# Optimization experiments

Hardware: AMD Instinct MI355X
Metric: run time of the kernel (lower is better)

Reference implementation:

```python
import jax, jax.numpy as jnp
import numpy as np
import math

PHI = (1 + math.sqrt(5)) / 2
ALPHA = 1 / PHI          # residual scale
BETA = 1 / PHI ** 2      # sparse-matmul scale
DIM = 1910
NZ = int(DIM * DIM / PHI)


def setup_inputs() -> dict:
    key = jax.random.key(0)
    kx, ki, kv = jax.random.split(key, 3)
    x = jax.random.normal(kx, (8, 4096, DIM), dtype=jnp.float32)
    W_indices = jax.random.randint(ki, (2, NZ), 0, DIM, dtype=jnp.int32)
    W_values = jax.random.normal(kv, (NZ,), dtype=jnp.float32) / math.sqrt(DIM)
    return {"x": x, "W_indices": W_indices, "W_values": W_values}


def reference(x, W_indices, W_values):
    dim = x.shape[-1]
    # COO -> dense: duplicate (row,col) entries sum, matching torch.sparse semantics.
    W = jnp.zeros((dim, dim), dtype=x.dtype).at[W_indices[0], W_indices[1]].add(W_values)
    orig_shape = x.shape
    xf = x.reshape(-1, dim)          # [tokens, dim]
    Wx = xf @ W.T                    # (W @ x.T).T == x @ W.T
    out = ALPHA * xf + BETA * Wx
    return out.reshape(orig_shape)
```

## Files before the change

### kernel.cpp

```cpp
#include <hip/hip_runtime.h>
#include <hip/hip_bf16.h>
#include <stdint.h>

#define DIMV 1910
#define KP   1920
#define NT   30
#define PHI_F  1.6180339887498949f
#define BETA_F 0.3819660112501051f

typedef __attribute__((ext_vector_type(4))) float f32x4;
typedef __attribute__((ext_vector_type(8))) short bf16x8;
typedef __attribute__((ext_vector_type(8))) unsigned short u16x8;

__device__ __forceinline__ void gl16(const void* g, void* l) {
    __builtin_amdgcn_global_load_lds(
        (const __attribute__((address_space(1))) void*)(uintptr_t)g,
        (__attribute__((address_space(3))) void*)(uint32_t)(uintptr_t)l,
        16, 0, 0);
}

__global__ void k_scatter(const int* __restrict__ ridx, const int* __restrict__ cidx,
                          const float* __restrict__ vals, float* __restrict__ Wd, int nz) {
    int i = blockIdx.x * 256 + threadIdx.x;
    if (i < nz) atomicAdd(Wd + (long)ridx[i] * DIMV + cidx[i], vals[i]);
}

__global__ void k_build_w(const float* __restrict__ Wd, unsigned short* __restrict__ Wb, int total8) {
    int stride = gridDim.x * blockDim.x;
    for (int i = blockIdx.x * blockDim.x + threadIdx.x; i < total8; i += stride) {
        int v = i * 8;
        int n = v / KP;
        int k = v - n * KP;
        u16x8 o;
#pragma unroll
        for (int j = 0; j < 8; ++j) {
            int kk = k + j;
            float fv = (n < DIMV && kk < DIMV) ? Wd[(size_t)n * DIMV + kk] : 0.f;
            if (kk == n && n < DIMV) fv += PHI_F;
            __hip_bfloat16 b = __float2bfloat16(fv);
            o[j] = *reinterpret_cast<unsigned short*>(&b);
        }
        *(u16x8*)(Wb + (size_t)v) = o;
    }
}

__global__ void k_conv_x(const float* __restrict__ x, unsigned short* __restrict__ xb, int total8) {
    int stride = gridDim.x * blockDim.x;
    for (int i = blockIdx.x * blockDim.x + threadIdx.x; i < total8; i += stride) {
        int v = i * 8;
        int row = v / KP;
        int col = v - row * KP;
        u16x8 o;
        if (col + 8 <= DIMV) {
            const float2* s = (const float2*)(x + (size_t)row * DIMV + col);
            float2 f0 = s[0], f1 = s[1], f2 = s[2], f3 = s[3];
            float f[8] = {f0.x, f0.y, f1.x, f1.y, f2.x, f2.y, f3.x, f3.y};
#pragma unroll
            for (int j = 0; j < 8; ++j) {
                __hip_bfloat16 b = __float2bfloat16(f[j]);
                o[j] = *reinterpret_cast<unsigned short*>(&b);
            }
        } else {
#pragma unroll
            for (int j = 0; j < 8; ++j) {
                int c = col + j;
                float fv = (c < DIMV) ? x[(size_t)row * DIMV + c] : 0.f;
                __hip_bfloat16 b = __float2bfloat16(fv);
                o[j] = *reinterpret_cast<unsigned short*>(&b);
            }
        }
        *(u16x8*)(xb + (size_t)v) = o;
    }
}

__global__ __launch_bounds__(512, 2) void k_gemm(const short* __restrict__ A,
                                                 const short* __restrict__ B,
                                                 float* __restrict__ C) {
    __shared__ char lds[131072];

    const int bid = blockIdx.x;
    const int bn  = bid & 7;
    const int bm  = bid >> 3;

    const int tid = threadIdx.x;
    const int w   = tid >> 6;
    const int l   = tid & 63;
    const int wm  = w >> 2;
    const int wn  = w & 3;
    const int fr  = l & 15;
    const int q   = l >> 4;

    const int    rs   = tid >> 3;
    const size_t KPB  = (size_t)KP * 2;
    const char*  aSrc = (const char*)A + (size_t)(bm * 256 + rs) * KPB + (((tid & 7) ^ (rs & 7)) * 16);
    const char*  bSrc = (const char*)B + (size_t)(bn * 256 + rs) * KPB + (((tid & 7) ^ (rs & 7)) * 16);
    char* stDst = lds + tid * 16;

    const int co0  = ((q    ) ^ (fr & 7)) * 16;
    const int co1  = ((4 + q) ^ (fr & 7)) * 16;
    const int aOff = (wm * 128 + fr) * 128;
    const int bOff = 32768 + (wn * 64 + fr) * 128;

    f32x4 acc[8][4] = {};

#define STAGE_A(tt, bo, s) gl16(aSrc + (size_t)(s) * 64 * KPB + (size_t)(tt) * 128, stDst + (bo) + (s) * 8192)
#define STAGE_B(tt, bo, s) gl16(bSrc + (size_t)(s) * 64 * KPB + (size_t)(tt) * 128, stDst + (bo) + 32768 + (s) * 8192)

#pragma unroll
    for (int s = 0; s < 4; ++s) STAGE_A(0, 0, s);
#pragma unroll
    for (int s = 0; s < 4; ++s) STAGE_B(0, 0, s);
    asm volatile("s_waitcnt vmcnt(0)" ::: "memory");
    __builtin_amdgcn_s_barrier();
    asm volatile("" ::: "memory");

    int bo = 0;
    for (int t = 0; t < NT; ++t) {
        const int nbo = bo ^ 65536;
        const char* pa = lds + bo + aOff;
        const char* pb = lds + bo + bOff;
        const bool st = (t + 1 < NT);
        bf16x8 a[4][2], b[2][2];

#pragma unroll
        for (int mi = 0; mi < 4; ++mi) {
            a[mi][0] = *(const bf16x8*)(pa + mi * 2048 + co0);
            a[mi][1] = *(const bf16x8*)(pa + mi * 2048 + co1);
        }
#pragma unroll
        for (int ni = 0; ni < 2; ++ni) {
            b[ni][0] = *(const bf16x8*)(pb + ni * 2048 + co0);
            b[ni][1] = *(const bf16x8*)(pb + ni * 2048 + co1);
        }
        if (st) { STAGE_A(t + 1, nbo, 0); STAGE_A(t + 1, nbo, 1); STAGE_A(t + 1, nbo, 2); }
        asm volatile("s_waitcnt lgkmcnt(8)" ::: "memory");
        __builtin_amdgcn_s_barrier();
        asm volatile("s_waitcnt lgkmcnt(0)" ::: "memory");
        __builtin_amdgcn_sched_barrier(0);
        __builtin_amdgcn_s_setprio(1);
#pragma unroll
        for (int kk = 0; kk < 2; ++kk)
#pragma unroll
            for (int mi = 0; mi < 4; ++mi)
#pragma unroll
                for (int ni = 0; ni < 2; ++ni)
                    acc[mi][ni] = __builtin_amdgcn_mfma_f32_16x16x32_bf16(a[mi][kk], b[ni][kk], acc[mi][ni], 0, 0, 0);
        __builtin_amdgcn_s_setprio(0);
        asm volatile("" ::: "memory");
        __builtin_amdgcn_s_barrier();
        asm volatile("" ::: "memory");

#pragma unroll
        for (int ni = 0; ni < 2; ++ni) {
            b[ni][0] = *(const bf16x8*)(pb + 4096 + ni * 2048 + co0);
            b[ni][1] = *(const bf16x8*)(pb + 4096 + ni * 2048 + co1);
        }
        if (st) { STAGE_A(t + 1, nbo, 3); STAGE_B(t + 1, nbo, 0); STAGE_B(t + 1, nbo, 1); }
        asm volatile("" ::: "memory");
        __builtin_amdgcn_s_barrier();
        asm volatile("s_waitcnt lgkmcnt(0)" ::: "memory");
        __builtin_amdgcn_sched_barrier(0);
        __builtin_amdgcn_s_setprio(1);
#pragma unroll
        for (int kk = 0; kk < 2; ++kk)
#pragma unroll
            for (int mi = 0; mi < 4; ++mi)
#pragma unroll
                for (int ni = 0; ni < 2; ++ni)
                    acc[mi][ni + 2] = __builtin_amdgcn_mfma_f32_16x16x32_bf16(a[mi][kk], b[ni][kk], acc[mi][ni + 2], 0, 0, 0);
        __builtin_amdgcn_s_setprio(0);
        asm volatile("" ::: "memory");
        __builtin_amdgcn_s_barrier();
        asm volatile("" ::: "memory");

#pragma unroll
        for (int mi = 0; mi < 4; ++mi) {
            a[mi][0] = *(const bf16x8*)(pa + 8192 + mi * 2048 + co0);
            a[mi][1] = *(const bf16x8*)(pa + 8192 + mi * 2048 + co1);
        }
        if (st) { STAGE_B(t + 1, nbo, 2); STAGE_B(t + 1, nbo, 3); }
        asm volatile("" ::: "memory");
        __builtin_amdgcn_s_barrier();
        asm volatile("s_waitcnt lgkmcnt(0)" ::: "memory");
        __builtin_amdgcn_sched_barrier(0);
        __builtin_amdgcn_s_setprio(1);
#pragma unroll
        for (int kk = 0; kk < 2; ++kk)
#pragma unroll
            for (int mi = 0; mi < 4; ++mi)
#pragma unroll
                for (int ni = 0; ni < 2; ++ni)
                    acc[mi + 4][ni + 2] = __builtin_amdgcn_mfma_f32_16x16x32_bf16(a[mi][kk], b[ni][kk], acc[mi + 4][ni + 2], 0, 0, 0);
        __builtin_amdgcn_s_setprio(0);
        asm volatile("" ::: "memory");
        __builtin_amdgcn_s_barrier();
        asm volatile("" ::: "memory");

#pragma unroll
        for (int ni = 0; ni < 2; ++ni) {
            b[ni][0] = *(const bf16x8*)(pb + ni * 2048 + co0);
            b[ni][1] = *(const bf16x8*)(pb + ni * 2048 + co1);
        }
        asm volatile("" ::: "memory");
        __builtin_amdgcn_s_barrier();
        asm volatile("s_waitcnt lgkmcnt(0)" ::: "memory");
        __builtin_amdgcn_sched_barrier(0);
        __builtin_amdgcn_s_setprio(1);
#pragma unroll
        for (int kk = 0; kk < 2; ++kk)
#pragma unroll
            for (int mi = 0; mi < 4; ++mi)
#pragma unroll
                for (int ni = 0; ni < 2; ++ni)
                    acc[mi + 4][ni] = __builtin_amdgcn_mfma_f32_16x16x32_bf16(a[mi][kk], b[ni][kk], acc[mi + 4][ni], 0, 0, 0);
        __builtin_amdgcn_s_setprio(0);
        asm volatile("s_waitcnt vmcnt(0)" ::: "memory");
        __builtin_amdgcn_s_barrier();
        asm volatile("" ::: "memory");

        bo = nbo;
    }
#undef STAGE_A
#undef STAGE_B

    const int grow0 = bm * 256 + wm * 128 + q * 4;
    const int gcol0 = bn * 256 + wn * 64 + fr;
#pragma unroll
    for (int mi = 0; mi < 8; ++mi) {
#pragma unroll
        for (int ni = 0; ni < 4; ++ni) {
            int gcol = gcol0 + ni * 16;
            if (gcol < DIMV) {
                size_t base = (size_t)(grow0 + mi * 16) * DIMV + gcol;
#pragma unroll
                for (int r = 0; r < 4; ++r)
                    C[base + (size_t)r * DIMV] = BETA_F * acc[mi][ni][r];
            }
        }
    }
}

extern "C" void kernel_launch(void* const* d_in, const int* in_sizes, int n_in,
                              void* d_out, int out_size, void* d_ws, size_t ws_size,
                              hipStream_t stream) {
    const float* x    = (const float*)d_in[0];
    const int*   widx = (const int*)d_in[1];
    const float* wval = (const float*)d_in[2];
    float* out = (float*)d_out;

    const int nz = in_sizes[2];
    const int M  = in_sizes[0] / DIMV;

    const size_t xb_bytes = (size_t)M * KP * 2;
    const size_t wb_bytes = (size_t)2048 * KP * 2;
    const size_t wd_bytes = (size_t)DIMV * DIMV * 4;
    char* ws = (char*)d_ws;
    unsigned short* xb = (unsigned short*)ws;
    unsigned short* Wb = (unsigned short*)(ws + xb_bytes);
    float*          Wd = (float*)ws;
    if (ws_size < xb_bytes + wb_bytes) return;
    (void)wd_bytes;

    hipMemsetAsync(Wd, 0, wd_bytes, stream);
    k_scatter<<<(nz + 255) / 256, 256, 0, stream>>>(widx, widx + nz, wval, Wd, nz);
    k_build_w<<<1800, 256, 0, stream>>>(Wd, Wb, KP * KP / 8);
    k_conv_x<<<2048, 256, 0, stream>>>(x, xb, M * KP / 8);
    k_gemm<<<1024, 512, 0, stream>>>((const short*)xb, (const short*)Wb, out);
}
```

Baseline: 473.7 us.

## Fuse fp32-to-bf16 x conversion into GEMM and make GEMM persistent over M tiles

Removes the separate k_conv_x pass and its bf16 workspace. The GEMM now loads fp32 x directly through registers, converts to bf16 and writes to LDS, so A staging no longer uses global_load_lds. The grid shrinks from 1024 to 256 blocks, and each block loops over 4 M tiles with the next tile's first K slice prefetched. This saves a full read/write of the 8x4096x1910 activation but adds VGPR pressure, register-path loads and longer per-block runtime with fewer blocks.

Result: slower. 620.0 us (+30.9%).

```diff
diff --git a/kernel.cpp b/kernel.cpp
--- a/kernel.cpp
+++ b/kernel.cpp
@@ -44,43 +44,14 @@
     }
 }
 
-__global__ void k_conv_x(const float* __restrict__ x, unsigned short* __restrict__ xb, int total8) {
-    int stride = gridDim.x * blockDim.x;
-    for (int i = blockIdx.x * blockDim.x + threadIdx.x; i < total8; i += stride) {
-        int v = i * 8;
-        int row = v / KP;
-        int col = v - row * KP;
-        u16x8 o;
-        if (col + 8 <= DIMV) {
-            const float2* s = (const float2*)(x + (size_t)row * DIMV + col);
-            float2 f0 = s[0], f1 = s[1], f2 = s[2], f3 = s[3];
-            float f[8] = {f0.x, f0.y, f1.x, f1.y, f2.x, f2.y, f3.x, f3.y};
-#pragma unroll
-            for (int j = 0; j < 8; ++j) {
-                __hip_bfloat16 b = __float2bfloat16(f[j]);
-                o[j] = *reinterpret_cast<unsigned short*>(&b);
-            }
-        } else {
-#pragma unroll
-            for (int j = 0; j < 8; ++j) {
-                int c = col + j;
-                float fv = (c < DIMV) ? x[(size_t)row * DIMV + c] : 0.f;
-                __hip_bfloat16 b = __float2bfloat16(fv);
-                o[j] = *reinterpret_cast<unsigned short*>(&b);
-            }
-        }
-        *(u16x8*)(xb + (size_t)v) = o;
-    }
-}
-
-__global__ __launch_bounds__(512, 2) void k_gemm(const short* __restrict__ A,
+__global__ __launch_bounds__(512, 2) void k_gemm(const float* __restrict__ X,
                                                  const short* __restrict__ B,
                                                  float* __restrict__ C) {
     __shared__ char lds[131072];
 
     const int bid = blockIdx.x;
     const int bn  = bid & 7;
-    const int bm  = bid >> 3;
+    const int bmg = bid >> 3;
 
     const int tid = threadIdx.x;
     const int w   = tid >> 6;
@@ -90,11 +61,12 @@
     const int fr  = l & 15;
     const int q   = l >> 4;
 
-    const int    rs   = tid >> 3;
+    const int    slot = tid & 7;
+    const int    srow = tid >> 3;
     const size_t KPB  = (size_t)KP * 2;
-    const char*  aSrc = (const char*)A + (size_t)(bm * 256 + rs) * KPB + (((tid & 7) ^ (rs & 7)) * 16);
-    const char*  bSrc = (const char*)B + (size_t)(bn * 256 + rs) * KPB + (((tid & 7) ^ (rs & 7)) * 16);
+    const char*  bSrc = (const char*)B + (size_t)(bn * 256 + srow) * KPB + (((tid & 7) ^ (srow & 7)) * 16);
     char* stDst = lds + tid * 16;
+    const int awOff = srow * 128 + ((slot ^ (srow & 7)) * 16);
 
     const int co0  = ((q    ) ^ (fr & 7)) * 16;
     const int co1  = ((4 + q) ^ (fr & 7)) * 16;
@@ -102,142 +74,211 @@
     const int bOff = 32768 + (wn * 64 + fr) * 128;
 
     f32x4 acc[8][4] = {};
-
-#define STAGE_A(tt, bo, s) gl16(aSrc + (size_t)(s) * 64 * KPB + (size_t)(tt) * 128, stDst + (bo) + (s) * 8192)
+    float2 av[4][4];
+
 #define STAGE_B(tt, bo, s) gl16(bSrc + (size_t)(s) * 64 * KPB + (size_t)(tt) * 128, stDst + (bo) + 32768 + (s) * 8192)
 
-#pragma unroll
-    for (int s = 0; s < 4; ++s) STAGE_A(0, 0, s);
-#pragma unroll
-    for (int s = 0; s < 4; ++s) STAGE_B(0, 0, s);
-    asm volatile("s_waitcnt vmcnt(0)" ::: "memory");
-    __builtin_amdgcn_s_barrier();
-    asm volatile("" ::: "memory");
-
-    int bo = 0;
-    for (int t = 0; t < NT; ++t) {
-        const int nbo = bo ^ 65536;
-        const char* pa = lds + bo + aOff;
-        const char* pb = lds + bo + bOff;
-        const bool st = (t + 1 < NT);
-        bf16x8 a[4][2], b[2][2];
-
-#pragma unroll
-        for (int mi = 0; mi < 4; ++mi) {
-            a[mi][0] = *(const bf16x8*)(pa + mi * 2048 + co0);
-            a[mi][1] = *(const bf16x8*)(pa + mi * 2048 + co1);
-        }
-#pragma unroll
-        for (int ni = 0; ni < 2; ++ni) {
-            b[ni][0] = *(const bf16x8*)(pb + ni * 2048 + co0);
-            b[ni][1] = *(const bf16x8*)(pb + ni * 2048 + co1);
-        }
-        if (st) { STAGE_A(t + 1, nbo, 0); STAGE_A(t + 1, nbo, 1); STAGE_A(t + 1, nbo, 2); }
-        asm volatile("s_waitcnt lgkmcnt(8)" ::: "memory");
-        __builtin_amdgcn_s_barrier();
+#define LOAD_A(xp, tts)                                                          \
+    {                                                                            \
+        const int c0 = (tts) * 64 + slot * 8;                                    \
+        if (__builtin_expect((tts) != NT - 1, 1)) {                              \
+            _Pragma("unroll")                                                    \
+            for (int s = 0; s < 4; ++s) {                                        \
+                const float* p = (xp) + (size_t)s * 64 * DIMV + c0;              \
+                av[s][0] = *(const float2*)(p);                                  \
+                av[s][1] = *(const float2*)(p + 2);                              \
+                av[s][2] = *(const float2*)(p + 4);                              \
+                av[s][3] = *(const float2*)(p + 6);                              \
+            }                                                                    \
+        } else {                                                                 \
+            _Pragma("unroll")                                                    \
+            for (int s = 0; s < 4; ++s) {                                        \
+                const float* p = (xp) + (size_t)s * 64 * DIMV;                   \
+                _Pragma("unroll")                                                \
+                for (int j = 0; j < 4; ++j) {                                    \
+                    int cp = c0 + j * 2;                                         \
+                    int cc = cp < (DIMV - 2) ? cp : (DIMV - 2);                  \
+                    float2 vv = *(const float2*)(p + cc);                        \
+                    if (cp >= DIMV) { vv.x = 0.f; vv.y = 0.f; }                  \
+                    av[s][j] = vv;                                               \
+                }                                                                \
+            }                                                                    \
+        }                                                                        \
+    }
+
+#define WRITE_A(bo)                                                              \
+    {                                                                            \
+        _Pragma("unroll")                                                        \
+        for (int s = 0; s < 4; ++s) {                                            \
+            u16x8 o;                                                             \
+            _Pragma("unroll")                                                    \
+            for (int j = 0; j < 4; ++j) {                                        \
+                __hip_bfloat16 b0 = __float2bfloat16(av[s][j].x);                \
+                __hip_bfloat16 b1 = __float2bfloat16(av[s][j].y);                \
+                o[j * 2]     = *reinterpret_cast<unsigned short*>(&b0);          \
+                o[j * 2 + 1] = *reinterpret_cast<unsigned short*>(&b1);          \
+            }                                                                    \
+            *(u16x8*)(lds + (bo) + s * 8192 + awOff) = o;                        \
+        }                                                                        \
+    }
+
+    {
+        const float* xp0 = X + ((size_t)(bmg * 256) + srow) * DIMV;
+        LOAD_A(xp0, 0)
+#pragma unroll
+        for (int s = 0; s < 4; ++s) STAGE_B(0, 0, s);
+        WRITE_A(0)
+        asm volatile("s_waitcnt vmcnt(0)" ::: "memory");
         asm volatile("s_waitcnt lgkmcnt(0)" ::: "memory");
-        __builtin_amdgcn_sched_barrier(0);
-        __builtin_amdgcn_s_setprio(1);
-#pragma unroll
-        for (int kk = 0; kk < 2; ++kk)
-#pragma unroll
-            for (int mi = 0; mi < 4; ++mi)
-#pragma unroll
-                for (int ni = 0; ni < 2; ++ni)
-                    acc[mi][ni] = __builtin_amdgcn_mfma_f32_16x16x32_bf16(a[mi][kk], b[ni][kk], acc[mi][ni], 0, 0, 0);
-        __builtin_amdgcn_s_setprio(0);
-        asm volatile("" ::: "memory");
         __builtin_amdgcn_s_barrier();
         asm volatile("" ::: "memory");
-
-#pragma unroll
-        for (int ni = 0; ni < 2; ++ni) {
-            b[ni][0] = *(const bf16x8*)(pb + 4096 + ni * 2048 + co0);
-            b[ni][1] = *(const bf16x8*)(pb + 4096 + ni * 2048 + co1);
+    }
+
+    for (int mt = 0; mt < 4; ++mt) {
+        const int bm = mt * 32 + bmg;
+        const float* pAm = X + ((size_t)(bm * 256) + srow) * DIMV;
+        int bo = 0;
+
+        for (int t = 0; t < NT; ++t) {
+            const int nbo = bo ^ 65536;
+            const char* pa = lds + bo + aOff;
+            const char* pb = lds + bo + bOff;
+            const bool st = (mt < 3) || (t + 1 < NT);
+            const int  tts = (t + 1 < NT) ? (t + 1) : 0;
+            const float* xp = (t + 1 < NT) ? pAm : pAm + (size_t)8192 * DIMV;
+            bf16x8 a[4][2], b[2][2];
+
+#pragma unroll
+            for (int mi = 0; mi < 4; ++mi) {
+                a[mi][0] = *(const bf16x8*)(pa + mi * 2048 + co0);
+                a[mi][1] = *(const bf16x8*)(pa + mi * 2048 + co1);
+            }
+#pragma unroll
+            for (int ni = 0; ni < 2; ++ni) {
+                b[ni][0] = *(const bf16x8*)(pb + ni * 2048 + co0);
+                b[ni][1] = *(const bf16x8*)(pb + ni * 2048 + co1);
+            }
+            if (st) LOAD_A(xp, tts)
+            asm volatile("s_waitcnt lgkmcnt(8)" ::: "memory");
+            __builtin_amdgcn_s_barrier();
+            asm volatile("s_waitcnt lgkmcnt(0)" ::: "memory");
+            __builtin_amdgcn_sched_barrier(0);
+            __builtin_amdgcn_s_setprio(1);
+#pragma unroll
+            for (int kk = 0; kk < 2; ++kk)
+#pragma unroll
+                for (int mi = 0; mi < 4; ++mi)
+#pragma unroll
+                    for (int ni = 0; ni < 2; ++ni)
+                        acc[mi][ni] = __builtin_amdgcn_mfma_f32_16x16x32_bf16(a[mi][kk], b[ni][kk], acc[mi][ni], 0, 0, 0);
+            __builtin_amdgcn_s_setprio(0);
+            asm volatile("" ::: "memory");
+            __builtin_amdgcn_s_barrier();
+            asm volatile("" ::: "memory");
+
+#pragma unroll
+            for (int ni = 0; ni < 2; ++ni) {
+                b[ni][0] = *(const bf16x8*)(pb + 4096 + ni * 2048 + co0);
+                b[ni][1] = *(const bf16x8*)(pb + 4096 + ni * 2048 + co1);
+            }
+            if (st) { STAGE_B(tts, nbo, 0); STAGE_B(tts, nbo, 1); }
+            asm volatile("" ::: "memory");
+            __builtin_amdgcn_s_barrier();
+            asm volatile("s_waitcnt lgkmcnt(0)" ::: "memory");
+            __builtin_amdgcn_sched_barrier(0);
+            __builtin_amdgcn_s_setprio(1);
+#pragma unroll
+            for (int kk = 0; kk < 2; ++kk)
+#pragma unroll
+                for (int mi = 0; mi < 4; ++mi)
+#pragma unroll
+                    for (int ni = 0; ni < 2; ++ni)
+                        acc[mi][ni + 2] = __builtin_amdgcn_mfma_f32_16x16x32_bf16(a[mi][kk], b[ni][kk], acc[mi][ni + 2], 0, 0, 0);
+            __builtin_amdgcn_s_setprio(0);
+            asm volatile("" ::: "memory");
+            __builtin_amdgcn_s_barrier();
+            asm volatile("" ::: "memory");
+
+#pragma unroll
+            for (int mi = 0; mi < 4; ++mi) {
+                a[mi][0] = *(const bf16x8*)(pa + 8192 + mi * 2048 + co0);
+                a[mi][1] = *(const bf16x8*)(pa + 8192 + mi * 2048 + co1);
+            }
+            if (st) {
+                STAGE_B(tts, nbo, 2); STAGE_B(tts, nbo, 3);
+                WRITE_A(nbo)
+            }
+            asm volatile("" ::: "memory");
+            __builtin_amdgcn_s_barrier();
+            asm volatile("s_waitcnt lgkmcnt(0)" ::: "memory");
+            __builtin_amdgcn_sched_barrier(0);
+            __builtin_amdgcn_s_setprio(1);
+#pragma unroll
+            for (int kk = 0; kk < 2; ++kk)
+#pragma unroll
+                for (int mi = 0; mi < 4; ++mi)
+#pragma unroll
+                    for (int ni = 0; ni < 2; ++ni)
+                        acc[mi + 4][ni + 2] = __builtin_amdgcn_mfma_f32_16x16x32_bf16(a[mi][kk], b[ni][kk], acc[mi + 4][ni + 2], 0, 0, 0);
+            __builtin_amdgcn_s_setprio(0);
+            asm volatile("" ::: "memory");
+            __builtin_amdgcn_s_barrier();
+            asm volatile("" ::: "memory");
+
+#pragma unroll
+            for (int ni = 0; ni < 2; ++ni) {
+                b[ni][0] = *(const bf16x8*)(pb + ni * 2048 + co0);
+                b[ni][1] = *(const bf16x8*)(pb + ni * 2048 + co1);
+            }
+            asm volatile("" ::: "memory");
+            __builtin_amdgcn_s_barrier();
+            asm volatile("s_waitcnt lgkmcnt(0)" ::: "memory");
+            __builtin_amdgcn_sched_barrier(0);
+            __builtin_amdgcn_s_setprio(1);
+#pragma unroll
+            for (int kk = 0; kk < 2; ++kk)
+#pragma unroll
+                for (int mi = 0; mi < 4; ++mi)
+#pragma unroll
+                    for (int ni = 0; ni < 2; ++ni)
+                        acc[mi + 4][ni] = __builtin_amdgcn_mfma_f32_16x16x32_bf16(a[mi][kk], b[ni][kk], acc[mi + 4][ni], 0, 0, 0);
+            __builtin_amdgcn_s_setprio(0);
+            asm volatile("s_waitcnt vmcnt(0)" ::: "memory");
+            __builtin_amdgcn_s_barrier();
+            asm volatile("" ::: "memory");
+
+            bo = nbo;
         }
-        if (st) { STAGE_A(t + 1, nbo, 3); STAGE_B(t + 1, nbo, 0); STAGE_B(t + 1, nbo, 1); }
-        asm volatile("" ::: "memory");
-        __builtin_amdgcn_s_barrier();
-        asm volatile("s_waitcnt lgkmcnt(0)" ::: "memory");
-        __builtin_amdgcn_sched_barrier(0);
-        __builtin_amdgcn_s_setprio(1);
-#pragma unroll
-        for (int kk = 0; kk < 2; ++kk)
-#pragma unroll
-            for (int mi = 0; mi < 4; ++mi)
-#pragma unroll
-                for (int ni = 0; ni < 2; ++ni)
-                    acc[mi][ni + 2] = __builtin_amdgcn_mfma_f32_16x16x32_bf16(a[mi][kk], b[ni][kk], acc[mi][ni + 2], 0, 0, 0);
-        __builtin_amdgcn_s_setprio(0);
-        asm volatile("" ::: "memory");
-        __builtin_amdgcn_s_barrier();
-        asm volatile("" ::: "memory");
-
-#pragma unroll
-        for (int mi = 0; mi < 4; ++mi) {
-            a[mi][0] = *(const bf16x8*)(pa + 8192 + mi * 2048 + co0);
-            a[mi][1] = *(const bf16x8*)(pa + 8192 + mi * 2048 + co1);
+
+        const int grow0 = bm * 256 + wm * 128 + q * 4;
+        const int gcol0 = bn * 256 + wn * 64 + fr;
+#pragma unroll
+        for (int ei = 0; ei < 8; ++ei) {
+#pragma unroll
+            for (int ni = 0; ni < 4; ++ni) {
+                int gcol = gcol0 + ni * 16;
+                if (gcol < DIMV) {
+                    size_t base = (size_t)(grow0 + ei * 16) * DIMV + gcol;
+#pragma unroll
+                    for (int r = 0; r < 4; ++r)
+                        C[base + (size_t)r * DIMV] = BETA_F * acc[ei][ni][r];
+                }
+            }
         }
-        if (st) { STAGE_B(t + 1, nbo, 2); STAGE_B(t + 1, nbo, 3); }
-        asm volatile("" ::: "memory");
-        __builtin_amdgcn_s_barrier();
-        asm volatile("s_waitcnt lgkmcnt(0)" ::: "memory");
-        __builtin_amdgcn_sched_barrier(0);
-        __builtin_amdgcn_s_setprio(1);
-#pragma unroll
-        for (int kk = 0; kk < 2; ++kk)
-#pragma unroll
-            for (int mi = 0; mi < 4; ++mi)
-#pragma unroll
-                for (int ni = 0; ni < 2; ++ni)
-                    acc[mi + 4][ni + 2] = __builtin_amdgcn_mfma_f32_16x16x32_bf16(a[mi][kk], b[ni][kk], acc[mi + 4][ni + 2], 0, 0, 0);
-        __builtin_amdgcn_s_setprio(0);
-        asm volatile("" ::: "memory");
-        __builtin_amdgcn_s_barrier();
-        asm volatile("" ::: "memory");
-
-#pragma unroll
-        for (int ni = 0; ni < 2; ++ni) {
-            b[ni][0] = *(const bf16x8*)(pb + ni * 2048 + co0);
-            b[ni][1] = *(const bf16x8*)(pb + ni * 2048 + co1);
+        if (mt < 3) {
+#pragma unroll
+            for (int ei = 0; ei < 8; ++ei)
+#pragma unroll
+                for (int ni = 0; ni < 4; ++ni)
+                    acc[ei][ni] = (f32x4)(0.f);
+            asm volatile("s_waitcnt vmcnt(0)" ::: "memory");
+            __builtin_amdgcn_s_barrier();
+            asm volatile("" ::: "memory");
         }
-        asm volatile("" ::: "memory");
-        __builtin_amdgcn_s_barrier();
-        asm volatile("s_waitcnt lgkmcnt(0)" ::: "memory");
-        __builtin_amdgcn_sched_barrier(0);
-        __builtin_amdgcn_s_setprio(1);
-#pragma unroll
-        for (int kk = 0; kk < 2; ++kk)
-#pragma unroll
-            for (int mi = 0; mi < 4; ++mi)
-#pragma unroll
-                for (int ni = 0; ni < 2; ++ni)
-                    acc[mi + 4][ni] = __builtin_amdgcn_mfma_f32_16x16x32_bf16(a[mi][kk], b[ni][kk], acc[mi + 4][ni], 0, 0, 0);
-        __builtin_amdgcn_s_setprio(0);
-        asm volatile("s_waitcnt vmcnt(0)" ::: "memory");
-        __builtin_amdgcn_s_barrier();
-        asm volatile("" ::: "memory");
-
-        bo = nbo;
-    }
-#undef STAGE_A
+    }
 #undef STAGE_B
-
-    const int grow0 = bm * 256 + wm * 128 + q * 4;
-    const int gcol0 = bn * 256 + wn * 64 + fr;
-#pragma unroll
-    for (int mi = 0; mi < 8; ++mi) {
-#pragma unroll
-        for (int ni = 0; ni < 4; ++ni) {
-            int gcol = gcol0 + ni * 16;
-            if (gcol < DIMV) {
-                size_t base = (size_t)(grow0 + mi * 16) * DIMV + gcol;
-#pragma unroll
-                for (int r = 0; r < 4; ++r)
-                    C[base + (size_t)r * DIMV] = BETA_F * acc[mi][ni][r];
-            }
-        }
-    }
+#undef LOAD_A
+#undef WRITE_A
 }
 
 extern "C" void kernel_launch(void* const* d_in, const int* in_sizes, int n_in,
@@ -249,21 +290,16 @@
     float* out = (float*)d_out;
 
     const int nz = in_sizes[2];
-    const int M  = in_sizes[0] / DIMV;
-
-    const size_t xb_bytes = (size_t)M * KP * 2;
+
     const size_t wb_bytes = (size_t)2048 * KP * 2;
     const size_t wd_bytes = (size_t)DIMV * DIMV * 4;
     char* ws = (char*)d_ws;
-    unsigned short* xb = (unsigned short*)ws;
-    unsigned short* Wb = (unsigned short*)(ws + xb_bytes);
-    float*          Wd = (float*)ws;
-    if (ws_size < xb_bytes + wb_bytes) return;
-    (void)wd_bytes;
+    unsigned short* Wb = (unsigned short*)ws;
+    float*          Wd = (float*)(ws + wb_bytes);
+    if (ws_size < wb_bytes + wd_bytes) return;
 
     hipMemsetAsync(Wd, 0, wd_bytes, stream);
     k_scatter<<<(nz + 255) / 256, 256, 0, stream>>>(widx, widx + nz, wval, Wd, nz);
     k_build_w<<<1800, 256, 0, stream>>>(Wd, Wb, KP * KP / 8);
-    k_conv_x<<<2048, 256, 0, stream>>>(x, xb, M * KP / 8);
-    k_gemm<<<1024, 512, 0, stream>>>((const short*)xb, (const short*)Wb, out);
-}
+    k_gemm<<<256, 512, 0, stream>>>(x, (const short*)Wb, out);
+}
```

## Fuse x conversion with COO scatter and make GEMM persistent over M tiles

Applied to the files above, without the earlier changes.

Merges the x-to-bf16 conversion and the atomic COO scatter into one kernel, with even blocks converting and odd blocks scattering, so the two prep stages run concurrently. The dense W scratch buffer is moved to its own workspace region so it no longer aliases xb. The GEMM now launches 256 blocks, each looping over 4 M tiles and prefetching the next tile's first A/B stage during the last K iteration of the current one, which hides the prologue load and cuts launch and tail waves. This trades parallelism (256 blocks at 2 per CU) for persistence, and the epilogue stores are no longer overlapped with another block's compute.

Result: faster. 399.2 us (-15.7%).

```diff
diff --git a/kernel.cpp b/kernel.cpp
--- a/kernel.cpp
+++ b/kernel.cpp
@@ -19,10 +19,43 @@
         16, 0, 0);
 }
 
-__global__ void k_scatter(const int* __restrict__ ridx, const int* __restrict__ cidx,
-                          const float* __restrict__ vals, float* __restrict__ Wd, int nz) {
-    int i = blockIdx.x * 256 + threadIdx.x;
-    if (i < nz) atomicAdd(Wd + (long)ridx[i] * DIMV + cidx[i], vals[i]);
+__global__ void k_prep(const float* __restrict__ x, unsigned short* __restrict__ xb, int total8,
+                       const int* __restrict__ ridx, const int* __restrict__ cidx,
+                       const float* __restrict__ vals, float* __restrict__ Wd, int nz) {
+    const int tid  = threadIdx.x;
+    const int half = (int)gridDim.x >> 1;
+    const int b    = (int)blockIdx.x >> 1;
+    const int stride = half * 256;
+    if ((blockIdx.x & 1) == 0) {
+        for (int i = b * 256 + tid; i < total8; i += stride) {
+            int v = i * 8;
+            int row = v / KP;
+            int col = v - row * KP;
+            u16x8 o;
+            if (col + 8 <= DIMV) {
+                const float2* s = (const float2*)(x + (size_t)row * DIMV + col);
+                float2 f0 = s[0], f1 = s[1], f2 = s[2], f3 = s[3];
+                float f[8] = {f0.x, f0.y, f1.x, f1.y, f2.x, f2.y, f3.x, f3.y};
+#pragma unroll
+                for (int j = 0; j < 8; ++j) {
+                    __hip_bfloat16 bb = __float2bfloat16(f[j]);
+                    o[j] = *reinterpret_cast<unsigned short*>(&bb);
+                }
+            } else {
+#pragma unroll
+                for (int j = 0; j < 8; ++j) {
+                    int c = col + j;
+                    float fv = (c < DIMV) ? x[(size_t)row * DIMV + c] : 0.f;
+                    __hip_bfloat16 bb = __float2bfloat16(fv);
+                    o[j] = *reinterpret_cast<unsigned short*>(&bb);
+                }
+            }
+            *(u16x8*)(xb + (size_t)v) = o;
+        }
+    } else {
+        for (int i = b * 256 + tid; i < nz; i += stride)
+            atomicAdd(Wd + (size_t)ridx[i] * DIMV + cidx[i], vals[i]);
+    }
 }
 
 __global__ void k_build_w(const float* __restrict__ Wd, unsigned short* __restrict__ Wb, int total8) {
@@ -44,35 +77,6 @@
     }
 }
 
-__global__ void k_conv_x(const float* __restrict__ x, unsigned short* __restrict__ xb, int total8) {
-    int stride = gridDim.x * blockDim.x;
-    for (int i = blockIdx.x * blockDim.x + threadIdx.x; i < total8; i += stride) {
-        int v = i * 8;
-        int row = v / KP;
-        int col = v - row * KP;
-        u16x8 o;
-        if (col + 8 <= DIMV) {
-            const float2* s = (const float2*)(x + (size_t)row * DIMV + col);
-            float2 f0 = s[0], f1 = s[1], f2 = s[2], f3 = s[3];
-            float f[8] = {f0.x, f0.y, f1.x, f1.y, f2.x, f2.y, f3.x, f3.y};
-#pragma unroll
-            for (int j = 0; j < 8; ++j) {
-                __hip_bfloat16 b = __float2bfloat16(f[j]);
-                o[j] = *reinterpret_cast<unsigned short*>(&b);
-            }
-        } else {
-#pragma unroll
-            for (int j = 0; j < 8; ++j) {
-                int c = col + j;
-                float fv = (c < DIMV) ? x[(size_t)row * DIMV + c] : 0.f;
-                __hip_bfloat16 b = __float2bfloat16(fv);
-                o[j] = *reinterpret_cast<unsigned short*>(&b);
-            }
-        }
-        *(u16x8*)(xb + (size_t)v) = o;
-    }
-}
-
 __global__ __launch_bounds__(512, 2) void k_gemm(const short* __restrict__ A,
                                                  const short* __restrict__ B,
                                                  float* __restrict__ C) {
@@ -80,7 +84,7 @@
 
     const int bid = blockIdx.x;
     const int bn  = bid & 7;
-    const int bm  = bid >> 3;
+    const int bmg = bid >> 3;
 
     const int tid = threadIdx.x;
     const int w   = tid >> 6;
@@ -90,10 +94,11 @@
     const int fr  = l & 15;
     const int q   = l >> 4;
 
-    const int    rs   = tid >> 3;
+    const int    srow = tid >> 3;
     const size_t KPB  = (size_t)KP * 2;
-    const char*  aSrc = (const char*)A + (size_t)(bm * 256 + rs) * KPB + (((tid & 7) ^ (rs & 7)) * 16);
-    const char*  bSrc = (const char*)B + (size_t)(bn * 256 + rs) * KPB + (((tid & 7) ^ (rs & 7)) * 16);
+    const int    swz  = ((tid & 7) ^ (srow & 7)) * 16;
+    const char*  aSrc0 = (const char*)A + (size_t)(bmg * 256 + srow) * KPB + swz;
+    const char*  bSrc  = (const char*)B + (size_t)(bn * 256 + srow) * KPB + swz;
     char* stDst = lds + tid * 16;
 
     const int co0  = ((q    ) ^ (fr & 7)) * 16;
@@ -103,141 +108,155 @@
 
     f32x4 acc[8][4] = {};
 
-#define STAGE_A(tt, bo, s) gl16(aSrc + (size_t)(s) * 64 * KPB + (size_t)(tt) * 128, stDst + (bo) + (s) * 8192)
-#define STAGE_B(tt, bo, s) gl16(bSrc + (size_t)(s) * 64 * KPB + (size_t)(tt) * 128, stDst + (bo) + 32768 + (s) * 8192)
-
-#pragma unroll
-    for (int s = 0; s < 4; ++s) STAGE_A(0, 0, s);
+#define STAGE_A(src, tt, bo, s) gl16((src) + (size_t)(s) * 64 * KPB + (size_t)(tt) * 128, stDst + (bo) + (s) * 8192)
+#define STAGE_B(tt, bo, s)      gl16(bSrc  + (size_t)(s) * 64 * KPB + (size_t)(tt) * 128, stDst + (bo) + 32768 + (s) * 8192)
+
+#pragma unroll
+    for (int s = 0; s < 4; ++s) STAGE_A(aSrc0, 0, 0, s);
 #pragma unroll
     for (int s = 0; s < 4; ++s) STAGE_B(0, 0, s);
     asm volatile("s_waitcnt vmcnt(0)" ::: "memory");
     __builtin_amdgcn_s_barrier();
     asm volatile("" ::: "memory");
 
-    int bo = 0;
-    for (int t = 0; t < NT; ++t) {
-        const int nbo = bo ^ 65536;
-        const char* pa = lds + bo + aOff;
-        const char* pb = lds + bo + bOff;
-        const bool st = (t + 1 < NT);
-        bf16x8 a[4][2], b[2][2];
-
-#pragma unroll
-        for (int mi = 0; mi < 4; ++mi) {
-            a[mi][0] = *(const bf16x8*)(pa + mi * 2048 + co0);
-            a[mi][1] = *(const bf16x8*)(pa + mi * 2048 + co1);
-        }
-#pragma unroll
-        for (int ni = 0; ni < 2; ++ni) {
-            b[ni][0] = *(const bf16x8*)(pb + ni * 2048 + co0);
-            b[ni][1] = *(const bf16x8*)(pb + ni * 2048 + co1);
-        }
-        if (st) { STAGE_A(t + 1, nbo, 0); STAGE_A(t + 1, nbo, 1); STAGE_A(t + 1, nbo, 2); }
-        asm volatile("s_waitcnt lgkmcnt(8)" ::: "memory");
-        __builtin_amdgcn_s_barrier();
-        asm volatile("s_waitcnt lgkmcnt(0)" ::: "memory");
-        __builtin_amdgcn_sched_barrier(0);
-        __builtin_amdgcn_s_setprio(1);
-#pragma unroll
-        for (int kk = 0; kk < 2; ++kk)
-#pragma unroll
-            for (int mi = 0; mi < 4; ++mi)
-#pragma unroll
-                for (int ni = 0; ni < 2; ++ni)
-                    acc[mi][ni] = __builtin_amdgcn_mfma_f32_16x16x32_bf16(a[mi][kk], b[ni][kk], acc[mi][ni], 0, 0, 0);
-        __builtin_amdgcn_s_setprio(0);
-        asm volatile("" ::: "memory");
-        __builtin_amdgcn_s_barrier();
-        asm volatile("" ::: "memory");
-
-#pragma unroll
-        for (int ni = 0; ni < 2; ++ni) {
-            b[ni][0] = *(const bf16x8*)(pb + 4096 + ni * 2048 + co0);
-            b[ni][1] = *(const bf16x8*)(pb + 4096 + ni * 2048 + co1);
-        }
-        if (st) { STAGE_A(t + 1, nbo, 3); STAGE_B(t + 1, nbo, 0); STAGE_B(t + 1, nbo, 1); }
-        asm volatile("" ::: "memory");
-        __builtin_amdgcn_s_barrier();
-        asm volatile("s_waitcnt lgkmcnt(0)" ::: "memory");
-        __builtin_amdgcn_sched_barrier(0);
-        __builtin_amdgcn_s_setprio(1);
-#pragma unroll
-        for (int kk = 0; kk < 2; ++kk)
-#pragma unroll
-            for (int mi = 0; mi < 4; ++mi)
-#pragma unroll
-                for (int ni = 0; ni < 2; ++ni)
-                    acc[mi][ni + 2] = __builtin_amdgcn_mfma_f32_16x16x32_bf16(a[mi][kk], b[ni][kk], acc[mi][ni + 2], 0, 0, 0);
-        __builtin_amdgcn_s_setprio(0);
-        asm volatile("" ::: "memory");
-        __builtin_amdgcn_s_barrier();
-        asm volatile("" ::: "memory");
-
-#pragma unroll
-        for (int mi = 0; mi < 4; ++mi) {
-            a[mi][0] = *(const bf16x8*)(pa + 8192 + mi * 2048 + co0);
-            a[mi][1] = *(const bf16x8*)(pa + 8192 + mi * 2048 + co1);
-        }
-        if (st) { STAGE_B(t + 1, nbo, 2); STAGE_B(t + 1, nbo, 3); }
-        asm volatile("" ::: "memory");
-        __builtin_amdgcn_s_barrier();
-        asm volatile("s_waitcnt lgkmcnt(0)" ::: "memory");
-        __builtin_amdgcn_sched_barrier(0);
-        __builtin_amdgcn_s_setprio(1);
-#pragma unroll
-        for (int kk = 0; kk < 2; ++kk)
-#pragma unroll
-            for (int mi = 0; mi < 4; ++mi)
-#pragma unroll
-                for (int ni = 0; ni < 2; ++ni)
-                    acc[mi + 4][ni + 2] = __builtin_amdgcn_mfma_f32_16x16x32_bf16(a[mi][kk], b[ni][kk], acc[mi + 4][ni + 2], 0, 0, 0);
-        __builtin_amdgcn_s_setprio(0);
-        asm volatile("" ::: "memory");
-        __builtin_amdgcn_s_barrier();
-        asm volatile("" ::: "memory");
-
-#pragma unroll
-        for (int ni = 0; ni < 2; ++ni) {
-            b[ni][0] = *(const bf16x8*)(pb + ni * 2048 + co0);
-            b[ni][1] = *(const bf16x8*)(pb + ni * 2048 + co1);
-        }
-        asm volatile("" ::: "memory");
-        __builtin_amdgcn_s_barrier();
-        asm volatile("s_waitcnt lgkmcnt(0)" ::: "memory");
-        __builtin_amdgcn_sched_barrier(0);
-        __builtin_amdgcn_s_setprio(1);
-#pragma unroll
-        for (int kk = 0; kk < 2; ++kk)
-#pragma unroll
-            for (int mi = 0; mi < 4; ++mi)
-#pragma unroll
-                for (int ni = 0; ni < 2; ++ni)
-                    acc[mi + 4][ni] = __builtin_amdgcn_mfma_f32_16x16x32_bf16(a[mi][kk], b[ni][kk], acc[mi + 4][ni], 0, 0, 0);
-        __builtin_amdgcn_s_setprio(0);
-        asm volatile("s_waitcnt vmcnt(0)" ::: "memory");
-        __builtin_amdgcn_s_barrier();
-        asm volatile("" ::: "memory");
-
-        bo = nbo;
+    for (int mt = 0; mt < 4; ++mt) {
+        const char* aSrc = aSrc0 + (size_t)mt * 8192 * KPB;
+        int bo = 0;
+
+        for (int t = 0; t < NT; ++t) {
+            const int nbo = bo ^ 65536;
+            const char* pa = lds + bo + aOff;
+            const char* pb = lds + bo + bOff;
+            const bool st  = (mt < 3) || (t + 1 < NT);
+            const int  tts = (t + 1 < NT) ? (t + 1) : 0;
+            const char* aS = (t + 1 < NT) ? aSrc : aSrc + (size_t)8192 * KPB;
+            bf16x8 a[4][2], b[2][2];
+
+#pragma unroll
+            for (int mi = 0; mi < 4; ++mi) {
+                a[mi][0] = *(const bf16x8*)(pa + mi * 2048 + co0);
+                a[mi][1] = *(const bf16x8*)(pa + mi * 2048 + co1);
+            }
+#pragma unroll
+            for (int ni = 0; ni < 2; ++ni) {
+                b[ni][0] = *(const bf16x8*)(pb + ni * 2048 + co0);
+                b[ni][1] = *(const bf16x8*)(pb + ni * 2048 + co1);
+            }
+            if (st) { STAGE_A(aS, tts, nbo, 0); STAGE_A(aS, tts, nbo, 1); STAGE_A(aS, tts, nbo, 2); }
+            asm volatile("s_waitcnt lgkmcnt(8)" ::: "memory");
+            __builtin_amdgcn_s_barrier();
+            asm volatile("s_waitcnt lgkmcnt(0)" ::: "memory");
+            __builtin_amdgcn_sched_barrier(0);
+            __builtin_amdgcn_s_setprio(1);
+#pragma unroll
+            for (int kk = 0; kk < 2; ++kk)
+#pragma unroll
+                for (int mi = 0; mi < 4; ++mi)
+#pragma unroll
+                    for (int ni = 0; ni < 2; ++ni)
+                        acc[mi][ni] = __builtin_amdgcn_mfma_f32_16x16x32_bf16(a[mi][kk], b[ni][kk], acc[mi][ni], 0, 0, 0);
+            __builtin_amdgcn_s_setprio(0);
+            asm volatile("" ::: "memory");
+            __builtin_amdgcn_s_barrier();
+            asm volatile("" ::: "memory");
+
+#pragma unroll
+            for (int ni = 0; ni < 2; ++ni) {
+                b[ni][0] = *(const bf16x8*)(pb + 4096 + ni * 2048 + co0);
+                b[ni][1] = *(const bf16x8*)(pb + 4096 + ni * 2048 + co1);
+            }
+            if (st) { STAGE_A(aS, tts, nbo, 3); STAGE_B(tts, nbo, 0); STAGE_B(tts, nbo, 1); }
+            asm volatile("" ::: "memory");
+            __builtin_amdgcn_s_barrier();
+            asm volatile("s_waitcnt lgkmcnt(0)" ::: "memory");
+            __builtin_amdgcn_sched_barrier(0);
+            __builtin_amdgcn_s_setprio(1);
+#pragma unroll
+            for (int kk = 0; kk < 2; ++kk)
+#pragma unroll
+                for (int mi = 0; mi < 4; ++mi)
+#pragma unroll
+                    for (int ni = 0; ni < 2; ++ni)
+                        acc[mi][ni + 2] = __builtin_amdgcn_mfma_f32_16x16x32_bf16(a[mi][kk], b[ni][kk], acc[mi][ni + 2], 0, 0, 0);
+            __builtin_amdgcn_s_setprio(0);
+            asm volatile("" ::: "memory");
+            __builtin_amdgcn_s_barrier();
+            asm volatile("" ::: "memory");
+
+#pragma unroll
+            for (int mi = 0; mi < 4; ++mi) {
+                a[mi][0] = *(const bf16x8*)(pa + 8192 + mi * 2048 + co0);
+                a[mi][1] = *(const bf16x8*)(pa + 8192 + mi * 2048 + co1);
+            }
+            if (st) { STAGE_B(tts, nbo, 2); STAGE_B(tts, nbo, 3); }
+            asm volatile("" ::: "memory");
+            __builtin_amdgcn_s_barrier();
+            asm volatile("s_waitcnt lgkmcnt(0)" ::: "memory");
+            __builtin_amdgcn_sched_barrier(0);
+            __builtin_amdgcn_s_setprio(1);
+#pragma unroll
+            for (int kk = 0; kk < 2; ++kk)
+#pragma unroll
+                for (int mi = 0; mi < 4; ++mi)
+#pragma unroll
+                    for (int ni = 0; ni < 2; ++ni)
+                        acc[mi + 4][ni + 2] = __builtin_amdgcn_mfma_f32_16x16x32_bf16(a[mi][kk], b[ni][kk], acc[mi + 4][ni + 2], 0, 0, 0);
+            __builtin_amdgcn_s_setprio(0);
+            asm volatile("" ::: "memory");
+            __builtin_amdgcn_s_barrier();
+            asm volatile("" ::: "memory");
+
+#pragma unroll
+            for (int ni = 0; ni < 2; ++ni) {
+                b[ni][0] = *(const bf16x8*)(pb + ni * 2048 + co0);
+                b[ni][1] = *(const bf16x8*)(pb + ni * 2048 + co1);
+            }
+            asm volatile("" ::: "memory");
+            __builtin_amdgcn_s_barrier();
+            asm volatile("s_waitcnt lgkmcnt(0)" ::: "memory");
+            __builtin_amdgcn_sched_barrier(0);
+            __builtin_amdgcn_s_setprio(1);
+#pragma unroll
+            for (int kk = 0; kk < 2; ++kk)
+#pragma unroll
+                for (int mi = 0; mi < 4; ++mi)
+#pragma unroll
+                    for (int ni = 0; ni < 2; ++ni)
+                        acc[mi + 4][ni] = __builtin_amdgcn_mfma_f32_16x16x32_bf16(a[mi][kk], b[ni][kk], acc[mi + 4][ni], 0, 0, 0);
+            __builtin_amdgcn_s_setprio(0);
+            asm volatile("s_waitcnt vmcnt(0)" ::: "memory");
+            __builtin_amdgcn_s_barrier();
+            asm volatile("" ::: "memory");
+
+            bo = nbo;
+        }
+
+        const int bm    = mt * 32 + bmg;
+        const int grow0 = bm * 256 + wm * 128 + q * 4;
+        const int gcol0 = bn * 256 + wn * 64 + fr;
+#pragma unroll
+        for (int ei = 0; ei < 8; ++ei) {
+#pragma unroll
+            for (int ni = 0; ni < 4; ++ni) {
+                int gcol = gcol0 + ni * 16;
+                if (gcol < DIMV) {
+                    size_t base = (size_t)(grow0 + ei * 16) * DIMV + gcol;
+#pragma unroll
+                    for (int r = 0; r < 4; ++r)
+                        C[base + (size_t)r * DIMV] = BETA_F * acc[ei][ni][r];
+                }
+            }
+        }
+        if (mt < 3) {
+#pragma unroll
+            for (int ei = 0; ei < 8; ++ei)
+#pragma unroll
+                for (int ni = 0; ni < 4; ++ni)
+                    acc[ei][ni] = (f32x4)(0.f);
+        }
     }
 #undef STAGE_A
 #undef STAGE_B
-
-    const int grow0 = bm * 256 + wm * 128 + q * 4;
-    const int gcol0 = bn * 256 + wn * 64 + fr;
-#pragma unroll
-    for (int mi = 0; mi < 8; ++mi) {
-#pragma unroll
-        for (int ni = 0; ni < 4; ++ni) {
-            int gcol = gcol0 + ni * 16;
-            if (gcol < DIMV) {
-                size_t base = (size_t)(grow0 + mi * 16) * DIMV + gcol;
-#pragma unroll
-                for (int r = 0; r < 4; ++r)
-                    C[base + (size_t)r * DIMV] = BETA_F * acc[mi][ni][r];
-            }
-        }
-    }
 }
 
 extern "C" void kernel_launch(void* const* d_in, const int* in_sizes, int n_in,
@@ -257,13 +276,11 @@
     char* ws = (char*)d_ws;
     unsigned short* xb = (unsigned short*)ws;
     unsigned short* Wb = (unsigned short*)(ws + xb_bytes);
-    float*          Wd = (float*)ws;
-    if (ws_size < xb_bytes + wb_bytes) return;
-    (void)wd_bytes;
+    float*          Wd = (float*)(ws + xb_bytes + wb_bytes);
+    if (ws_size < xb_bytes + wb_bytes + wd_bytes) return;
 
     hipMemsetAsync(Wd, 0, wd_bytes, stream);
-    k_scatter<<<(nz + 255) / 256, 256, 0, stream>>>(widx, widx + nz, wval, Wd, nz);
+    k_prep<<<2048, 256, 0, stream>>>(x, xb, M * KP / 8, widx, widx + nz, wval, Wd, nz);
     k_build_w<<<1800, 256, 0, stream>>>(Wd, Wb, KP * KP / 8);
-    k_conv_x<<<2048, 256, 0, stream>>>(x, xb, M * KP / 8);
-    k_gemm<<<1024, 512, 0, stream>>>((const short*)xb, (const short*)Wb, out);
-}
+    k_gemm<<<256, 512, 0, stream>>>((const short*)xb, (const short*)Wb, out);
+}
```
